# Kernel optimization log

Hardware: AMD Instinct MI355X
Metric: run time of the kernel (lower is better)

## Reference

```python
import jax, jax.numpy as jnp
import numpy as np

N = 100_000   # nodes
E = 800_000   # edges
F_IN = 128    # num_features
E_IN = 64     # edge_dim
H = 100       # n_hidden
L = 2         # num_gnn_layers
BN_EPS = 1e-5


def _lin(key, fan_in, fan_out, extra=()):
    kw, _ = jax.random.split(key)
    w = jax.random.normal(kw, (*extra, fan_in, fan_out), jnp.float32) / np.float32(np.sqrt(fan_in))
    b = jnp.zeros((*extra, fan_out), jnp.float32)
    return w, b


def setup_inputs() -> dict:
    key = jax.random.key(0)
    ks = jax.random.split(key, 12)
    x = jax.random.normal(ks[0], (N, F_IN), jnp.float32)
    edge_index = jax.random.randint(ks[1], (2, E), 0, N, dtype=jnp.int32)
    edge_attr = jax.random.normal(ks[2], (E, E_IN), jnp.float32)
    node_w, node_b = _lin(ks[3], F_IN, H)
    edge_w, edge_b = _lin(ks[4], E_IN, H)
    lin_w, lin_b = _lin(ks[5], H, H, (L,))   # GINEConv edge lin per layer
    w1, b1 = _lin(ks[6], H, H, (L,))         # GINEConv nn first Linear
    w2, b2 = _lin(ks[7], H, H, (L,))         # GINEConv nn second Linear
    gamma = jnp.ones((L, H), jnp.float32)
    beta = jnp.zeros((L, H), jnp.float32)
    ew1, eb1 = _lin(ks[8], 3 * H, H, (L,))   # edge-update MLP
    ew2, eb2 = _lin(ks[9], H, H, (L,))
    mw1, mb1 = _lin(ks[10], 3 * H, 50)
    k11, k12 = jax.random.split(ks[11])
    mw2, mb2 = _lin(k11, 50, 25)
    mw3, mb3 = _lin(k12, 25, 2)
    return dict(x=x, edge_index=edge_index, edge_attr=edge_attr,
                node_w=node_w, node_b=node_b, edge_w=edge_w, edge_b=edge_b,
                lin_w=lin_w, lin_b=lin_b, w1=w1, b1=b1, w2=w2, b2=b2,
                gamma=gamma, beta=beta, ew1=ew1, eb1=eb1, ew2=ew2, eb2=eb2,
                mw1=mw1, mb1=mb1, mw2=mw2, mb2=mb2, mw3=mw3, mb3=mb3)


def reference(x, edge_index, edge_attr, node_w, node_b, edge_w, edge_b,
              lin_w, lin_b, w1, b1, w2, b2, gamma, beta,
              ew1, eb1, ew2, eb2, mw1, mb1, mw2, mb2, mw3, mb3):
    src, dst = edge_index[0], edge_index[1]
    h = x @ node_w + node_b          # [N, H]
    e = edge_attr @ edge_w + edge_b  # [E, H]
    for i in range(L):
        # GINEConv: message = relu(x_src + lin(edge_attr)); sum-aggregate at dst
        msg = jax.nn.relu(h[src] + (e @ lin_w[i] + lin_b[i]))       # [E, H]
        agg = jax.ops.segment_sum(msg, dst, num_segments=N)         # [N, H]
        z = h + agg                                                  # (1+eps)*x + aggr, eps=0
        z = jax.nn.relu(z @ w1[i] + b1[i]) @ w2[i] + b2[i]
        # BatchNorm over nodes (training mode, biased variance)
        mu = z.mean(0)
        var = z.var(0)
        z = (z - mu) * jax.lax.rsqrt(var + BN_EPS) * gamma[i] + beta[i]
        h = (h + jax.nn.relu(z)) / 2
        # edge update: emlp(cat(x_src, x_dst, e))
        cat = jnp.concatenate([h[src], h[dst], e], axis=-1)         # [E, 3H]
        e = e + (jax.nn.relu(cat @ ew1[i] + eb1[i]) @ ew2[i] + eb2[i]) / 2
    feat = jnp.concatenate(
        [jax.nn.relu(jnp.concatenate([h[src], h[dst]], axis=-1)), e], axis=1)  # [E, 3H]
    out = jax.nn.relu(feat @ mw1 + mb1)
    out = jax.nn.relu(out @ mw2 + mb2)
    return out @ mw3 + mb3  # [E, 2]
```

## Files before the change

### kernel.cpp

```cpp
#include <hip/hip_runtime.h>

#define N_NODES 100000
#define N_EDGES 800000
#define HDIM 100
#define LDP 112
#define TSTR 104

typedef __attribute__((ext_vector_type(8))) short bf16x8;
typedef __attribute__((ext_vector_type(4))) float f32x4;

__device__ inline uint packsplit(float v) {
    uint u = __float_as_uint(v);
    float r = v - __uint_as_float(u & 0xFFFF0000u);
    return (u & 0xFFFF0000u) | (__float_as_uint(r) >> 16);
}
__device__ inline float recw(uint w) {
    return __uint_as_float(w & 0xFFFF0000u) + __uint_as_float(w << 16);
}
__device__ inline uint4 relu4(uint4 a) {
    a.x &= ~(uint)((int)a.x >> 31); a.y &= ~(uint)((int)a.y >> 31);
    a.z &= ~(uint)((int)a.z >> 31); a.w &= ~(uint)((int)a.w >> 31);
    return a;
}
__device__ inline void unpack16(uint4 a, uint4 b, bf16x8& h8, bf16x8& l8) {
    union { uint u[4]; bf16x8 v; } H, L;
    H.u[0] = __builtin_amdgcn_perm(a.y, a.x, 0x07060302u);
    H.u[1] = __builtin_amdgcn_perm(a.w, a.z, 0x07060302u);
    H.u[2] = __builtin_amdgcn_perm(b.y, b.x, 0x07060302u);
    H.u[3] = __builtin_amdgcn_perm(b.w, b.z, 0x07060302u);
    L.u[0] = __builtin_amdgcn_perm(a.y, a.x, 0x05040100u);
    L.u[1] = __builtin_amdgcn_perm(a.w, a.z, 0x05040100u);
    L.u[2] = __builtin_amdgcn_perm(b.y, b.x, 0x05040100u);
    L.u[3] = __builtin_amdgcn_perm(b.w, b.z, 0x05040100u);
    h8 = H.v; l8 = L.v;
}
__device__ inline void split8(float4 a, float4 b, bf16x8& h8, bf16x8& l8) {
    float v[8] = {a.x, a.y, a.z, a.w, b.x, b.y, b.z, b.w};
    bf16x8 hh, ll;
#pragma unroll
    for (int i = 0; i < 8; ++i) {
        uint u = __float_as_uint(v[i]);
        hh[i] = (short)(u >> 16);
        float r = v[i] - __uint_as_float(u & 0xFFFF0000u);
        ll[i] = (short)(__float_as_uint(r) >> 16);
    }
    h8 = hh; l8 = ll;
}

template<int CONCAT>
__global__ __launch_bounds__(256)
void pack_k(const float* __restrict__ W, ushort* __restrict__ hi, ushort* __restrict__ lo,
            int K, int NC, int Kpad, int NCpad, int total)
{
    int idx = blockIdx.x * 256 + threadIdx.x;
    if (idx >= total) return;
    int per = NCpad * Kpad;
    int b = idx / per, rem = idx - b * per;
    int col = rem / Kpad, kv = rem - col * Kpad;
    int srck; bool valid;
    if (CONCAT) {
        int seg = kv >> 7, off = kv & 127;
        srck = seg * 100 + off;
        valid = (off < 100) && (srck < K) && (col < NC);
    } else {
        srck = kv;
        valid = (kv < K) && (col < NC);
    }
    float v = valid ? W[(long)b * K * NC + (long)srck * NC + col] : 0.f;
    uint w = packsplit(v);
    hi[idx] = (ushort)(w >> 16);
    lo[idx] = (ushort)(w & 0xFFFFu);
}

template<int TILES, int TPW, int STEPS, int MODE, int GATHER, int AFP32, int OUTF32, int CLAMP>
__global__ __launch_bounds__(256, 2)
void gemm9_k(const uint* aP, int lda, const float* __restrict__ aF, int ldaf,
             const ushort* __restrict__ wH, const ushort* __restrict__ wL,
             const float* __restrict__ bias,
             float* __restrict__ Cf, uint* cP, int ldc,
             int M, int NC, const int* __restrict__ g0)
{
    constexpr int KPADW = STEPS * 32;
    const int tid  = threadIdx.x;
    const int lane = tid & 63;
    const int w    = tid >> 6;
    const int cl   = lane & 15;
    const int kgrp = lane >> 4;
    const long row0 = (long)blockIdx.x * 64;

    int arows[4];
#pragma unroll
    for (int rg = 0; rg < 4; ++rg) {
        long grow = row0 + rg * 16 + cl;
        int gc = (int)((grow < M) ? grow : (M - 1));
        arows[rg] = (GATHER == 3) ? g0[gc] : gc;
    }

    uint4  aw0[2][4], aw1[2][4];
    float4 af0[2][4], af1[2][4];
    bf16x8 bh[2][TPW], bl[2][TPW];
    f32x4  acc[TPW][4];
#pragma unroll
    for (int tp = 0; tp < TPW; ++tp)
#pragma unroll
        for (int rg = 0; rg < 4; ++rg) acc[tp][rg] = (f32x4){0.f, 0.f, 0.f, 0.f};

    auto loadA = [&](int st, int sl) {
        const int kk = st * 32 + kgrp * 8;
#pragma unroll
        for (int rg = 0; rg < 4; ++rg) {
            if (AFP32) {
                const float* p = aF + (size_t)arows[rg] * ldaf + kk;
                af0[sl][rg] = *(const float4*)p;
                af1[sl][rg] = *(const float4*)(p + 4);
            } else {
                bool ok = !CLAMP || ((st & 3) != 3) || (kgrp == 0);
                if (ok) {
                    const uint* p = aP + (size_t)arows[rg] * lda + kk;
                    aw0[sl][rg] = *(const uint4*)p;
                    aw1[sl][rg] = *(const uint4*)(p + 4);
                } else {
                    aw0[sl][rg] = make_uint4(0, 0, 0, 0);
                    aw1[sl][rg] = make_uint4(0, 0, 0, 0);
                }
            }
        }
    };
    auto loadB = [&](int st, int sl) {
        int kk = st * 32 + kgrp * 8;
#pragma unroll
        for (int tp = 0; tp < TPW; ++tp) {
            int colw = (w * TPW + tp) * 16 + cl;
            bh[sl][tp] = *(const bf16x8*)(wH + (size_t)colw * KPADW + kk);
            bl[sl][tp] = *(const bf16x8*)(wL + (size_t)colw * KPADW + kk);
        }
    };

    loadA(0, 0); loadB(0, 0);
    if (STEPS > 1) { loadA(1, 1); loadB(1, 1); }

#pragma unroll
    for (int st = 0; st < STEPS; ++st) {
        const int sl = st & 1;
#pragma unroll
        for (int rg = 0; rg < 4; ++rg) {
            bf16x8 aH, aL;
            if (AFP32) split8(af0[sl][rg], af1[sl][rg], aH, aL);
            else       unpack16(aw0[sl][rg], aw1[sl][rg], aH, aL);
#pragma unroll
            for (int tp = 0; tp < TPW; ++tp) {
                acc[tp][rg] = __builtin_amdgcn_mfma_f32_16x16x32_bf16(aL, bh[sl][tp], acc[tp][rg], 0, 0, 0);
                acc[tp][rg] = __builtin_amdgcn_mfma_f32_16x16x32_bf16(aH, bl[sl][tp], acc[tp][rg], 0, 0, 0);
                acc[tp][rg] = __builtin_amdgcn_mfma_f32_16x16x32_bf16(aH, bh[sl][tp], acc[tp][rg], 0, 0, 0);
            }
        }
        if (st + 2 < STEPS) { loadA(st + 2, sl); loadB(st + 2, sl); }
    }

#pragma unroll
    for (int tp = 0; tp < TPW; ++tp) {
        int col = (w * TPW + tp) * 16 + cl;
        if (col >= NC) continue;
        float bv = bias[col];
#pragma unroll
        for (int rg = 0; rg < 4; ++rg) {
#pragma unroll
            for (int i = 0; i < 4; ++i) {
                long grow = row0 + rg * 16 + kgrp * 4 + i;
                if (grow >= M) continue;
                float v = acc[tp][rg][i] + bv;
                if (MODE == 1) v = fmaxf(v, 0.f);
                long o = grow * (long)ldc + col;
                if (OUTF32) Cf[o] = v;
                else        cP[o] = packsplit(v);
            }
        }
    }
}

__global__ __launch_bounds__(256, 2)
void msg_agg_k(const uint* __restrict__ eP,
               const ushort* __restrict__ wH, const ushort* __restrict__ wL,
               const float* __restrict__ bias,
               const uint* __restrict__ hP,
               const int* __restrict__ psrc, const int* __restrict__ pdst,
               float* __restrict__ aggF)
{
    __shared__ float sm[64 * 108];
    __shared__ int sd[64];
    const int tid = threadIdx.x, lane = tid & 63, w = tid >> 6;
    const int cl = lane & 15, kgrp = lane >> 4;
    const long row0 = (long)blockIdx.x * 64;

    if (tid < 64) sd[tid] = pdst[row0 + tid];

    int sr[4][4];
#pragma unroll
    for (int rg = 0; rg < 4; ++rg)
#pragma unroll
        for (int i = 0; i < 4; ++i)
            sr[rg][i] = psrc[row0 + rg * 16 + kgrp * 4 + i];

    uint4 aw0[2][4], aw1[2][4];
    bf16x8 bh[2][2], bl[2][2];
    f32x4 acc[2][4];
#pragma unroll
    for (int tp = 0; tp < 2; ++tp)
#pragma unroll
        for (int rg = 0; rg < 4; ++rg) acc[tp][rg] = (f32x4){0.f, 0.f, 0.f, 0.f};

    auto loadA = [&](int st, int sl) {
        const int kk = st * 32 + kgrp * 8;
        bool ok = ((st & 3) != 3) || (kgrp == 0);
#pragma unroll
        for (int rg = 0; rg < 4; ++rg) {
            if (ok) {
                const uint* p = eP + (size_t)(row0 + rg * 16 + cl) * LDP + kk;
                aw0[sl][rg] = *(const uint4*)p;
                aw1[sl][rg] = *(const uint4*)(p + 4);
            } else {
                aw0[sl][rg] = make_uint4(0, 0, 0, 0);
                aw1[sl][rg] = make_uint4(0, 0, 0, 0);
            }
        }
    };
    auto loadB = [&](int st, int sl) {
        int kk = st * 32 + kgrp * 8;
#pragma unroll
        for (int tp = 0; tp < 2; ++tp) {
            int colw = (w * 2 + tp) * 16 + cl;
            bh[sl][tp] = *(const bf16x8*)(wH + (size_t)colw * 128 + kk);
            bl[sl][tp] = *(const bf16x8*)(wL + (size_t)colw * 128 + kk);
        }
    };

    loadA(0, 0); loadB(0, 0); loadA(1, 1); loadB(1, 1);
#pragma unroll
    for (int st = 0; st < 4; ++st) {
        const int sl = st & 1;
#pragma unroll
        for (int rg = 0; rg < 4; ++rg) {
            bf16x8 aH, aL;
            unpack16(aw0[sl][rg], aw1[sl][rg], aH, aL);
#pragma unroll
            for (int tp = 0; tp < 2; ++tp) {
                acc[tp][rg] = __builtin_amdgcn_mfma_f32_16x16x32_bf16(aL, bh[sl][tp], acc[tp][rg], 0, 0, 0);
                acc[tp][rg] = __builtin_amdgcn_mfma_f32_16x16x32_bf16(aH, bl[sl][tp], acc[tp][rg], 0, 0, 0);
                acc[tp][rg] = __builtin_amdgcn_mfma_f32_16x16x32_bf16(aH, bh[sl][tp], acc[tp][rg], 0, 0, 0);
            }
        }
        if (st + 2 < 4) { loadA(st + 2, sl); loadB(st + 2, sl); }
    }

#pragma unroll
    for (int tp = 0; tp < 2; ++tp) {
        int col = (w * 2 + tp) * 16 + cl;
        if (col < 100) {
            float bv = bias[col];
#pragma unroll
            for (int rg = 0; rg < 4; ++rg)
#pragma unroll
                for (int i = 0; i < 4; ++i) {
                    int row = rg * 16 + kgrp * 4 + i;
                    float hv = recw(hP[(size_t)sr[rg][i] * LDP + col]);
                    sm[row * 108 + col] = fmaxf(acc[tp][rg][i] + bv + hv, 0.f);
                }
        }
    }
    __syncthreads();

    if (tid < 100) {
        const int c = tid;
        int cur = sd[0];
        float s = 0.f;
        bool first = true;
        for (int r = 0; r < 64; ++r) {
            int d = sd[r];
            if (d != cur) {
                bool contPrev = first && (row0 > 0) && (pdst[row0 - 1] == cur);
                if (contPrev) atomicAdd(&aggF[(size_t)cur * TSTR + c], s);
                else aggF[(size_t)cur * TSTR + c] = recw(hP[(size_t)cur * LDP + c]) + s;
                first = false; s = 0.f; cur = d;
            }
            s += sm[r * 108 + c];
        }
        bool contPrev = first && (row0 > 0) && (pdst[row0 - 1] == cur);
        bool contNext = (row0 + 64 < N_EDGES) && (pdst[row0 + 64] == cur);
        if (contPrev || contNext) atomicAdd(&aggF[(size_t)cur * TSTR + c], s);
        else aggF[(size_t)cur * TSTR + c] = recw(hP[(size_t)cur * LDP + c]) + s;
    }
}

__global__ __launch_bounds__(256, 2)
void fused_edge_k(const uint* __restrict__ hP, uint* eP,
                  const ushort* __restrict__ w1H, const ushort* __restrict__ w1L,
                  const float* __restrict__ b1v,
                  const ushort* __restrict__ w2H, const ushort* __restrict__ w2L,
                  const float* __restrict__ b2v,
                  const int* __restrict__ g0, const int* __restrict__ g1)
{
    __shared__ uint sm[64 * 108];
    const int tid = threadIdx.x, lane = tid & 63, w = tid >> 6;
    const int cl = lane & 15, kgrp = lane >> 4;
    const long row0 = (long)blockIdx.x * 64;

    int rs[4], rd[4];
#pragma unroll
    for (int rg = 0; rg < 4; ++rg) {
        long gr = row0 + rg * 16 + cl;
        rs[rg] = g0[gr]; rd[rg] = g1[gr];
    }

    uint4 aw0[2][4], aw1[2][4];
    bf16x8 bh[2][2], bl[2][2];
    f32x4 acc[2][4];
#pragma unroll
    for (int tp = 0; tp < 2; ++tp)
#pragma unroll
        for (int rg = 0; rg < 4; ++rg) acc[tp][rg] = (f32x4){0.f, 0.f, 0.f, 0.f};

    auto loadA = [&](int st, int sl) {
        int seg = st >> 2, inseg = (st & 3) * 32 + kgrp * 8;
        bool ok = ((st & 3) != 3) || (kgrp == 0);
        const uint* base = (seg == 2) ? eP : hP;
#pragma unroll
        for (int rg = 0; rg < 4; ++rg) {
            if (ok) {
                long row = (seg == 0) ? rs[rg] : (seg == 1) ? rd[rg] : (row0 + rg * 16 + cl);
                const uint* p = base + (size_t)row * LDP + inseg;
                aw0[sl][rg] = *(const uint4*)p;
                aw1[sl][rg] = *(const uint4*)(p + 4);
            } else {
                aw0[sl][rg] = make_uint4(0, 0, 0, 0);
                aw1[sl][rg] = make_uint4(0, 0, 0, 0);
            }
        }
    };
    auto loadB = [&](int st, int sl) {
        int kk = st * 32 + kgrp * 8;
#pragma unroll
        for (int tp = 0; tp < 2; ++tp) {
            int colw = (w * 2 + tp) * 16 + cl;
            bh[sl][tp] = *(const bf16x8*)(w1H + (size_t)colw * 384 + kk);
            bl[sl][tp] = *(const bf16x8*)(w1L + (size_t)colw * 384 + kk);
        }
    };

    loadA(0, 0); loadB(0, 0); loadA(1, 1); loadB(1, 1);
#pragma unroll
    for (int st = 0; st < 12; ++st) {
        const int sl = st & 1;
#pragma unroll
        for (int rg = 0; rg < 4; ++rg) {
            bf16x8 aH, aL;
            unpack16(aw0[sl][rg], aw1[sl][rg], aH, aL);
#pragma unroll
            for (int tp = 0; tp < 2; ++tp) {
                acc[tp][rg] = __builtin_amdgcn_mfma_f32_16x16x32_bf16(aL, bh[sl][tp], acc[tp][rg], 0, 0, 0);
                acc[tp][rg] = __builtin_amdgcn_mfma_f32_16x16x32_bf16(aH, bl[sl][tp], acc[tp][rg], 0, 0, 0);
                acc[tp][rg] = __builtin_amdgcn_mfma_f32_16x16x32_bf16(aH, bh[sl][tp], acc[tp][rg], 0, 0, 0);
            }
        }
        if (st + 2 < 12) { loadA(st + 2, sl); loadB(st + 2, sl); }
    }

#pragma unroll
    for (int tp = 0; tp < 2; ++tp) {
        int col = (w * 2 + tp) * 16 + cl;
        if (col < 108) {
            float bv = (col < 100) ? b1v[col] : 0.f;
#pragma unroll
            for (int rg = 0; rg < 4; ++rg)
#pragma unroll
                for (int i = 0; i < 4; ++i) {
                    int row = rg * 16 + kgrp * 4 + i;
                    uint u = 0;
                    if (col < 100) u = packsplit(fmaxf(acc[tp][rg][i] + bv, 0.f));
                    sm[row * 108 + col] = u;
                }
        }
    }
    __syncthreads();

    f32x4 acc2[2][4];
#pragma unroll
    for (int tp = 0; tp < 2; ++tp)
#pragma unroll
        for (int rg = 0; rg < 4; ++rg) acc2[tp][rg] = (f32x4){0.f, 0.f, 0.f, 0.f};
    bf16x8 ch[2][2], clo[2][2];
    auto loadB2 = [&](int st, int sl) {
        int kk = st * 32 + kgrp * 8;
#pragma unroll
        for (int tp = 0; tp < 2; ++tp) {
            int colw = (w * 2 + tp) * 16 + cl;
            ch[sl][tp]  = *(const bf16x8*)(w2H + (size_t)colw * 128 + kk);
            clo[sl][tp] = *(const bf16x8*)(w2L + (size_t)colw * 128 + kk);
        }
    };
    loadB2(0, 0); loadB2(1, 1);
#pragma unroll
    for (int st = 0; st < 4; ++st) {
        const int sl = st & 1;
#pragma unroll
        for (int rg = 0; rg < 4; ++rg) {
            int row = rg * 16 + cl;
            int kk = st * 32 + kgrp * 8;
            uint4 q0 = make_uint4(0, 0, 0, 0), q1 = make_uint4(0, 0, 0, 0);
            if ((st != 3) || (kgrp == 0)) {
                q0 = *(const uint4*)&sm[row * 108 + kk];
                q1 = *(const uint4*)&sm[row * 108 + kk + 4];
            }
            bf16x8 aH, aL;
            unpack16(q0, q1, aH, aL);
#pragma unroll
            for (int tp = 0; tp < 2; ++tp) {
                acc2[tp][rg] = __builtin_amdgcn_mfma_f32_16x16x32_bf16(aL, ch[sl][tp], acc2[tp][rg], 0, 0, 0);
                acc2[tp][rg] = __builtin_amdgcn_mfma_f32_16x16x32_bf16(aH, clo[sl][tp], acc2[tp][rg], 0, 0, 0);
                acc2[tp][rg] = __builtin_amdgcn_mfma_f32_16x16x32_bf16(aH, ch[sl][tp], acc2[tp][rg], 0, 0, 0);
            }
        }
        if (st + 2 < 4) loadB2(st + 2, sl);
    }
#pragma unroll
    for (int tp = 0; tp < 2; ++tp) {
        int col = (w * 2 + tp) * 16 + cl;
        if (col >= 100) continue;
        float bv = b2v[col];
#pragma unroll
        for (int rg = 0; rg < 4; ++rg)
#pragma unroll
            for (int i = 0; i < 4; ++i) {
                long grow = row0 + rg * 16 + kgrp * 4 + i;
                long o = grow * (long)LDP + col;
                float v = recw(eP[o]) + 0.5f * (acc2[tp][rg][i] + bv);
                eP[o] = packsplit(v);
            }
    }
}

__global__ __launch_bounds__(256, 2)
void fused_final_k(const uint* __restrict__ hP, const uint* __restrict__ eP,
                   const ushort* __restrict__ m1H, const ushort* __restrict__ m1L,
                   const float* __restrict__ mb1,
                   const ushort* __restrict__ m2H, const ushort* __restrict__ m2L,
                   const float* __restrict__ mb2, const float* __restrict__ mw3,
                   const float* __restrict__ mb3,
                   const int* __restrict__ g0, const int* __restrict__ g1,
                   const int* __restrict__ eidx, float* __restrict__ out)
{
    __shared__ uint sm[64 * 68];
    const int tid = threadIdx.x, lane = tid & 63, w = tid >> 6;
    const int cl = lane & 15, kgrp = lane >> 4;
    const long row0 = (long)blockIdx.x * 64;

    int rs[4], rd[4];
#pragma unroll
    for (int rg = 0; rg < 4; ++rg) {
        long gr = row0 + rg * 16 + cl;
        rs[rg] = g0[gr]; rd[rg] = g1[gr];
    }

    uint4 aw0[2][4], aw1[2][4];
    bf16x8 bh[2], bl[2];
    f32x4 acc1[4];
#pragma unroll
    for (int rg = 0; rg < 4; ++rg) acc1[rg] = (f32x4){0.f, 0.f, 0.f, 0.f};

    auto loadA = [&](int st, int sl) {
        int seg = st >> 2, inseg = (st & 3) * 32 + kgrp * 8;
        bool ok = ((st & 3) != 3) || (kgrp == 0);
        const uint* base = (seg == 2) ? eP : hP;
#pragma unroll
        for (int rg = 0; rg < 4; ++rg) {
            if (ok) {
                long row = (seg == 0) ? rs[rg] : (seg == 1) ? rd[rg] : (row0 + rg * 16 + cl);
                const uint* p = base + (size_t)row * LDP + inseg;
                aw0[sl][rg] = *(const uint4*)p;
                aw1[sl][rg] = *(const uint4*)(p + 4);
            } else {
                aw0[sl][rg] = make_uint4(0, 0, 0, 0);
                aw1[sl][rg] = make_uint4(0, 0, 0, 0);
            }
        }
    };
    auto loadB = [&](int st, int sl) {
        int kk = st * 32 + kgrp * 8;
        int colw = w * 16 + cl;
        bh[sl] = *(const bf16x8*)(m1H + (size_t)colw * 384 + kk);
        bl[sl] = *(const bf16x8*)(m1L + (size_t)colw * 384 + kk);
    };

    loadA(0, 0); loadB(0, 0); loadA(1, 1); loadB(1, 1);
#pragma unroll
    for (int st = 0; st < 12; ++st) {
        const int sl = st & 1;
#pragma unroll
        for (int rg = 0; rg < 4; ++rg) {
            uint4 w0 = aw0[sl][rg], w1 = aw1[sl][rg];
            if (st < 8) { w0 = relu4(w0); w1 = relu4(w1); }
            bf16x8 aH, aL;
            unpack16(w0, w1, aH, aL);
            acc1[rg] = __builtin_amdgcn_mfma_f32_16x16x32_bf16(aL, bh[sl], acc1[rg], 0, 0, 0);
            acc1[rg] = __builtin_amdgcn_mfma_f32_16x16x32_bf16(aH, bl[sl], acc1[rg], 0, 0, 0);
            acc1[rg] = __builtin_amdgcn_mfma_f32_16x16x32_bf16(aH, bh[sl], acc1[rg], 0, 0, 0);
        }
        if (st + 2 < 12) { loadA(st + 2, sl); loadB(st + 2, sl); }
    }

    {
        int col = w * 16 + cl;
        float bv = (col < 50) ? mb1[col] : 0.f;
#pragma unroll
        for (int rg = 0; rg < 4; ++rg)
#pragma unroll
            for (int i = 0; i < 4; ++i) {
                int row = rg * 16 + kgrp * 4 + i;
                uint u = 0;
                if (col < 50) u = packsplit(fmaxf(acc1[rg][i] + bv, 0.f));
                sm[row * 68 + col] = u;
            }
    }
    __syncthreads();

    bf16x8 c2h[2][2], c2l[2][2];
#pragma unroll
    for (int t = 0; t < 2; ++t)
#pragma unroll
        for (int st = 0; st < 2; ++st) {
            long o = (long)(t * 16 + cl) * 64 + st * 32 + kgrp * 8;
            c2h[t][st] = *(const bf16x8*)(m2H + o);
            c2l[t][st] = *(const bf16x8*)(m2L + o);
        }
    const float bias0 = mb2[cl];
    const float bias1 = (cl + 16 < 25) ? mb2[cl + 16] : 0.f;
    const float w3a0 = mw3[cl * 2 + 0], w3a1 = mw3[cl * 2 + 1];
    const float w3b0 = (cl + 16 < 25) ? mw3[(cl + 16) * 2 + 0] : 0.f;
    const float w3b1 = (cl + 16 < 25) ? mw3[(cl + 16) * 2 + 1] : 0.f;
    const float b30 = mb3[0], b31 = mb3[1];

    const int row = w * 16 + cl;
    f32x4 a0 = (f32x4){0.f, 0.f, 0.f, 0.f}, a1 = a0;
#pragma unroll
    for (int st = 0; st < 2; ++st) {
        int kk = st * 32 + kgrp * 8;
        uint4 q0 = *(const uint4*)&sm[row * 68 + kk];
        uint4 q1 = *(const uint4*)&sm[row * 68 + kk + 4];
        bf16x8 aH, aL;
        unpack16(q0, q1, aH, aL);
        a0 = __builtin_amdgcn_mfma_f32_16x16x32_bf16(aL, c2h[0][st], a0, 0, 0, 0);
        a0 = __builtin_amdgcn_mfma_f32_16x16x32_bf16(aH, c2l[0][st], a0, 0, 0, 0);
        a0 = __builtin_amdgcn_mfma_f32_16x16x32_bf16(aH, c2h[0][st], a0, 0, 0, 0);
        a1 = __builtin_amdgcn_mfma_f32_16x16x32_bf16(aL, c2h[1][st], a1, 0, 0, 0);
        a1 = __builtin_amdgcn_mfma_f32_16x16x32_bf16(aH, c2l[1][st], a1, 0, 0, 0);
        a1 = __builtin_amdgcn_mfma_f32_16x16x32_bf16(aH, c2h[1][st], a1, 0, 0, 0);
    }
#pragma unroll
    for (int i = 0; i < 4; ++i) {
        float t0 = fmaxf(a0[i] + bias0, 0.f);
        float t1 = fmaxf(a1[i] + bias1, 0.f);
        float s0 = t0 * w3a0 + t1 * w3b0;
        float s1 = t0 * w3a1 + t1 * w3b1;
#pragma unroll
        for (int d = 1; d < 16; d <<= 1) {
            s0 += __shfl_xor(s0, d, 64);
            s1 += __shfl_xor(s1, d, 64);
        }
        if (cl == 0) {
            long grow = row0 + w * 16 + kgrp * 4 + i;
            int oe = eidx[grow];
            out[(long)oe * 2 + 0] = s0 + b30;
            out[(long)oe * 2 + 1] = s1 + b31;
        }
    }
}

__global__ __launch_bounds__(256)
void hist_k(const int* __restrict__ dst, int* __restrict__ cnt)
{
    int e = blockIdx.x * 256 + threadIdx.x;
    if (e < N_EDGES) atomicAdd(&cnt[dst[e]], 1);
}

__global__ __launch_bounds__(1024)
void scan_k(const int* __restrict__ cnt, int* __restrict__ off)
{
    __shared__ int part[1024];
    const int t = threadIdx.x;
    const int per = (N_NODES + 1023) / 1024;
    const int base = t * per;
    int s = 0;
    for (int i = 0; i < per; ++i) {
        int n = base + i;
        if (n < N_NODES) s += cnt[n];
    }
    part[t] = s;
    __syncthreads();
    for (int d = 1; d < 1024; d <<= 1) {
        int v = (t >= d) ? part[t - d] : 0;
        __syncthreads();
        part[t] += v;
        __syncthreads();
    }
    int run = (t == 0) ? 0 : part[t - 1];
    for (int i = 0; i < per; ++i) {
        int n = base + i;
        if (n < N_NODES) { off[n] = run; run += cnt[n]; }
    }
    if (t == 1023) off[N_NODES] = run;
}

__global__ __launch_bounds__(256)
void fill_k(const int* __restrict__ dst, const int* __restrict__ off,
            int* __restrict__ pos, int* __restrict__ eidx)
{
    int e = blockIdx.x * 256 + threadIdx.x;
    if (e >= N_EDGES) return;
    int d = dst[e];
    int p = atomicAdd(&pos[d], 1);
    eidx[off[d] + p] = e;
}

__global__ __launch_bounds__(256)
void perm_k(const int* __restrict__ eidx, const int* __restrict__ src,
            const int* __restrict__ dst, int* __restrict__ psrc, int* __restrict__ pdst)
{
    int j = blockIdx.x * 256 + threadIdx.x;
    if (j >= N_EDGES) return;
    int e = eidx[j];
    psrc[j] = src[e];
    pdst[j] = dst[e];
}

__global__ __launch_bounds__(256)
void h2agg_k(const uint* __restrict__ hP, float* __restrict__ aggF)
{
    unsigned idx = blockIdx.x * 256u + threadIdx.x;
    if (idx >= (unsigned)(N_NODES * 26)) return;
    unsigned n = idx / 26u;
    unsigned q = (idx - n * 26u) * 4u;
    long ob = (long)n * TSTR + q;
    if (q >= 100) {
        *(float4*)&aggF[ob] = make_float4(0.f, 0.f, 0.f, 0.f);
        return;
    }
    uint4 hw = *(const uint4*)&hP[(long)n * LDP + q];
    *(float4*)&aggF[ob] = make_float4(recw(hw.x), recw(hw.y), recw(hw.z), recw(hw.w));
}

__global__ __launch_bounds__(128)
void bn_stats_k(const float* __restrict__ z, float* __restrict__ stats)
{
    int c = threadIdx.x;
    if (c >= HDIM) return;
    long rows_per = (N_NODES + gridDim.x - 1) / gridDim.x;
    long r0 = (long)blockIdx.x * rows_per;
    long r1 = r0 + rows_per; if (r1 > N_NODES) r1 = N_NODES;
    float s = 0.f, s2 = 0.f;
    for (long r = r0; r < r1; ++r) {
        float v = z[r * TSTR + c];
        s += v; s2 += v * v;
    }
    atomicAdd(&stats[c], s);
    atomicAdd(&stats[HDIM + c], s2);
}

__global__ __launch_bounds__(256)
void bn_apply_k(const float* __restrict__ z2, const float* __restrict__ stats,
                const float* __restrict__ gamma, const float* __restrict__ beta,
                uint* __restrict__ hP)
{
    unsigned idx = blockIdx.x * 256u + threadIdx.x;
    if (idx >= (unsigned)(N_NODES * 25)) return;
    unsigned n = idx / 25u;
    unsigned q = (idx - n * 25u) * 4u;
    const float invN = 1.f / N_NODES;
    long ob = (long)n * LDP + q;
    uint4 hw = *(const uint4*)&hP[ob];
    float4 zv = *(const float4*)&z2[(long)n * TSTR + q];
    float hv[4] = {recw(hw.x), recw(hw.y), recw(hw.z), recw(hw.w)};
    float zz[4] = {zv.x, zv.y, zv.z, zv.w};
    float r[4];
#pragma unroll
    for (int i = 0; i < 4; ++i) {
        unsigned c = q + i;
        float mu  = stats[c] * invN;
        float var = stats[HDIM + c] * invN - mu * mu;
        float v = (zz[i] - mu) * rsqrtf(var + 1e-5f) * gamma[c] + beta[c];
        r[i] = (hv[i] + fmaxf(v, 0.f)) * 0.5f;
    }
    *(uint4*)&hP[ob] = make_uint4(packsplit(r[0]), packsplit(r[1]), packsplit(r[2]), packsplit(r[3]));
}

static inline int gb64(long m) { return (int)((m + 63) / 64); }

extern "C" void kernel_launch(void* const* d_in, const int* in_sizes, int n_in,
                              void* d_out, int out_size, void* d_ws, size_t ws_size,
                              hipStream_t stream)
{
    const float* x         = (const float*)d_in[0];
    const int*   ei        = (const int*)  d_in[1];
    const float* edge_attr = (const float*)d_in[2];
    const float* node_w    = (const float*)d_in[3];
    const float* node_b    = (const float*)d_in[4];
    const float* edge_w    = (const float*)d_in[5];
    const float* edge_b    = (const float*)d_in[6];
    const float* lin_w     = (const float*)d_in[7];
    const float* lin_b     = (const float*)d_in[8];
    const float* w1        = (const float*)d_in[9];
    const float* b1        = (const float*)d_in[10];
    const float* w2        = (const float*)d_in[11];
    const float* b2        = (const float*)d_in[12];
    const float* gamma     = (const float*)d_in[13];
    const float* beta      = (const float*)d_in[14];
    const float* ew1       = (const float*)d_in[15];
    const float* eb1       = (const float*)d_in[16];
    const float* ew2       = (const float*)d_in[17];
    const float* eb2       = (const float*)d_in[18];
    const float* mw1       = (const float*)d_in[19];
    const float* mb1       = (const float*)d_in[20];
    const float* mw2       = (const float*)d_in[21];
    const float* mb2       = (const float*)d_in[22];
    const float* mw3       = (const float*)d_in[23];
    const float* mb3       = (const float*)d_in[24];
    float* out = (float*)d_out;

    ushort* pw = (ushort*)d_ws;
    size_t off_w = 0;
    ushort *nwH, *nwL, *ewH, *ewL, *liH, *liL, *w1H, *w1L, *w2H, *w2L,
           *e1H, *e1L, *e2H, *e2L, *m1H, *m1L, *m2H, *m2L;
    auto nextw = [&](size_t s, ushort*& H, ushort*& L) { H = pw + off_w; L = pw + off_w + s; off_w += 2 * s; };
    nextw(128 * 128,     nwH, nwL);
    nextw(128 * 64,      ewH, ewL);
    nextw(2 * 128 * 128, liH, liL);
    nextw(2 * 128 * 128, w1H, w1L);
    nextw(2 * 128 * 128, w2H, w2L);
    nextw(2 * 128 * 384, e1H, e1L);
    nextw(2 * 128 * 128, e2H, e2L);
    nextw(64 * 384,      m1H, m1L);
    nextw(32 * 64,       m2H, m2L);

    int* intb = (int*)((char*)d_ws + (2u << 20));
    int* cnt   = intb;
    int* coff  = cnt + N_NODES;
    int* pos   = coff + N_NODES + 1;
    int* eidx  = pos + N_NODES;
    int* psrc  = eidx + N_EDGES;
    int* pdst  = psrc + N_EDGES;
    float* stats = (float*)(pdst + N_EDGES);

    char* fbase = (char*)d_ws + (16u << 20);
    uint* eP = (uint*)fbase;
    uint* hP = eP + (size_t)N_EDGES * LDP;
    uint* zP = hP + (size_t)N_NODES * LDP;
    char* big = (char*)(zP + (size_t)N_NODES * LDP);
    float* aggF = (float*)big;
    float* z2   = aggF + (size_t)N_NODES * TSTR;

    const int* srcp = ei;
    const int* dstp = ei + N_EDGES;
    dim3 blk(256);

    auto packl = [&](const float* W, ushort* H, ushort* L, int K, int NC, int Kp, int NCp, int batch, bool cc) {
        int total = batch * NCp * Kp;
        if (cc) pack_k<1><<<(total + 255) / 256, blk, 0, stream>>>(W, H, L, K, NC, Kp, NCp, total);
        else    pack_k<0><<<(total + 255) / 256, blk, 0, stream>>>(W, H, L, K, NC, Kp, NCp, total);
    };
    packl(node_w, nwH, nwL, 128, 100, 128, 128, 1, false);
    packl(edge_w, ewH, ewL,  64, 100,  64, 128, 1, false);
    packl(lin_w,  liH, liL, 100, 100, 128, 128, 2, false);
    packl(w1,     w1H, w1L, 100, 100, 128, 128, 2, false);
    packl(w2,     w2H, w2L, 100, 100, 128, 128, 2, false);
    packl(ew1,    e1H, e1L, 300, 100, 384, 128, 2, true);
    packl(ew2,    e2H, e2L, 100, 100, 128, 128, 2, false);
    packl(mw1,    m1H, m1L, 300,  50, 384,  64, 1, true);
    packl(mw2,    m2H, m2L,  50,  25,  64,  32, 1, false);

    hipMemsetAsync(cnt, 0, N_NODES * sizeof(int), stream);
    hist_k<<<(N_EDGES + 255) / 256, blk, 0, stream>>>(dstp, cnt);
    scan_k<<<1, dim3(1024), 0, stream>>>(cnt, coff);
    hipMemsetAsync(pos, 0, N_NODES * sizeof(int), stream);
    fill_k<<<(N_EDGES + 255) / 256, blk, 0, stream>>>(dstp, coff, pos, eidx);
    perm_k<<<(N_EDGES + 255) / 256, blk, 0, stream>>>(eidx, srcp, dstp, psrc, pdst);

    gemm9_k<8,2,4,0,0,1,0,0><<<gb64(N_NODES), blk, 0, stream>>>(
        nullptr, 0, x, 128, nwH, nwL, node_b, nullptr, hP, LDP, N_NODES, 100, nullptr);
    gemm9_k<8,2,2,0,3,1,0,0><<<gb64(N_EDGES), blk, 0, stream>>>(
        nullptr, 0, edge_attr, 64, ewH, ewL, edge_b, nullptr, eP, LDP, N_EDGES, 100, eidx);

    for (int i = 0; i < 2; ++i) {
        h2agg_k<<<(N_NODES * 26 + 255) / 256, blk, 0, stream>>>(hP, aggF);
        msg_agg_k<<<gb64(N_EDGES), blk, 0, stream>>>(
            eP, liH + (size_t)i * 16384, liL + (size_t)i * 16384, lin_b + i * HDIM,
            hP, psrc, pdst, aggF);
        gemm9_k<8,2,4,1,0,1,0,0><<<gb64(N_NODES), blk, 0, stream>>>(
            nullptr, 0, aggF, TSTR, w1H + (size_t)i * 16384, w1L + (size_t)i * 16384,
            b1 + i * HDIM, nullptr, zP, LDP, N_NODES, 100, nullptr);
        gemm9_k<8,2,4,0,0,0,1,1><<<gb64(N_NODES), blk, 0, stream>>>(
            zP, LDP, nullptr, 0, w2H + (size_t)i * 16384, w2L + (size_t)i * 16384,
            b2 + i * HDIM, z2, nullptr, TSTR, N_NODES, 100, nullptr);
        hipMemsetAsync(stats, 0, 2 * HDIM * sizeof(float), stream);
        bn_stats_k<<<1024, dim3(128), 0, stream>>>(z2, stats);
        bn_apply_k<<<(N_NODES * 25 + 255) / 256, blk, 0, stream>>>(
            z2, stats, gamma + i * HDIM, beta + i * HDIM, hP);
        fused_edge_k<<<gb64(N_EDGES), blk, 0, stream>>>(
            hP, eP,
            e1H + (size_t)i * 49152, e1L + (size_t)i * 49152, eb1 + i * HDIM,
            e2H + (size_t)i * 16384, e2L + (size_t)i * 16384, eb2 + i * HDIM,
            psrc, pdst);
    }

    fused_final_k<<<gb64(N_EDGES), blk, 0, stream>>>(
        hP, eP, m1H, m1L, mb1, m2H, m2L, mb2, mw3, mb3, psrc, pdst, eidx, out);
}
```

Baseline: 3.550 ms.

## Precompute per-node projections of src/dst blocks for edge MLP first layer

The first linear layer of the edge-update MLP and the final MLP is split by input block. The h[src] and h[dst] parts are computed once per node (N rows) into PSD/QSD tables, and the edge kernels only run a K=100 GEMM on the edge features plus two gathered adds. This removes two-thirds of the per-edge MFMA work and the gathered reads of full hidden rows, at the cost of extra node-level GEMM launches, new buffers and gathers from the projection tables. The relu on concatenated h in the final head is moved into the node GEMM through a new RELUA template flag.

Result: faster. 3.435 ms (-3.2%).

```diff
diff --git a/kernel.cpp b/kernel.cpp
--- a/kernel.cpp
+++ b/kernel.cpp
@@ -5,6 +5,9 @@
 #define HDIM 100
 #define LDP 112
 #define TSTR 104
+#define TS 108
+#define PSTR 224
+#define QSTR 128
 
 typedef __attribute__((ext_vector_type(8))) short bf16x8;
 typedef __attribute__((ext_vector_type(4))) float f32x4;
@@ -47,38 +50,29 @@
     h8 = hh; l8 = ll;
 }
 
-template<int CONCAT>
 __global__ __launch_bounds__(256)
 void pack_k(const float* __restrict__ W, ushort* __restrict__ hi, ushort* __restrict__ lo,
-            int K, int NC, int Kpad, int NCpad, int total)
+            int K, int NC, int Kpad, int NCpad, int total, int krow0, int srcK)
 {
     int idx = blockIdx.x * 256 + threadIdx.x;
     if (idx >= total) return;
     int per = NCpad * Kpad;
     int b = idx / per, rem = idx - b * per;
     int col = rem / Kpad, kv = rem - col * Kpad;
-    int srck; bool valid;
-    if (CONCAT) {
-        int seg = kv >> 7, off = kv & 127;
-        srck = seg * 100 + off;
-        valid = (off < 100) && (srck < K) && (col < NC);
-    } else {
-        srck = kv;
-        valid = (kv < K) && (col < NC);
-    }
-    float v = valid ? W[(long)b * K * NC + (long)srck * NC + col] : 0.f;
+    bool valid = (kv < K) && (col < NC);
+    float v = valid ? W[(long)b * srcK * NC + (long)(krow0 + kv) * NC + col] : 0.f;
     uint w = packsplit(v);
     hi[idx] = (ushort)(w >> 16);
     lo[idx] = (ushort)(w & 0xFFFFu);
 }
 
-template<int TILES, int TPW, int STEPS, int MODE, int GATHER, int AFP32, int OUTF32, int CLAMP>
+template<int TILES, int TPW, int STEPS, int MODE, int GATHER, int AFP32, int OUTF32, int CLAMP, int RELUA>
 __global__ __launch_bounds__(256, 2)
-void gemm9_k(const uint* aP, int lda, const float* __restrict__ aF, int ldaf,
-             const ushort* __restrict__ wH, const ushort* __restrict__ wL,
-             const float* __restrict__ bias,
-             float* __restrict__ Cf, uint* cP, int ldc,
-             int M, int NC, const int* __restrict__ g0)
+void gemm10_k(const uint* aP, int lda, const float* __restrict__ aF, int ldaf,
+              const ushort* __restrict__ wH, const ushort* __restrict__ wL,
+              const float* __restrict__ bias,
+              float* __restrict__ Cf, uint* cP, int ldc,
+              int M, int NC, const int* __restrict__ g0)
 {
     constexpr int KPADW = STEPS * 32;
     const int tid  = threadIdx.x;
@@ -146,7 +140,11 @@
         for (int rg = 0; rg < 4; ++rg) {
             bf16x8 aH, aL;
             if (AFP32) split8(af0[sl][rg], af1[sl][rg], aH, aL);
-            else       unpack16(aw0[sl][rg], aw1[sl][rg], aH, aL);
+            else {
+                uint4 q0 = aw0[sl][rg], q1 = aw1[sl][rg];
+                if (RELUA) { q0 = relu4(q0); q1 = relu4(q1); }
+                unpack16(q0, q1, aH, aL);
+            }
 #pragma unroll
             for (int tp = 0; tp < TPW; ++tp) {
                 acc[tp][rg] = __builtin_amdgcn_mfma_f32_16x16x32_bf16(aL, bh[sl][tp], acc[tp][rg], 0, 0, 0);
@@ -186,20 +184,14 @@
                const int* __restrict__ psrc, const int* __restrict__ pdst,
                float* __restrict__ aggF)
 {
-    __shared__ float sm[64 * 108];
-    __shared__ int sd[64];
+    __shared__ float sm[64 * TS];
+    __shared__ int sd[64], ssr[64];
     const int tid = threadIdx.x, lane = tid & 63, w = tid >> 6;
     const int cl = lane & 15, kgrp = lane >> 4;
     const long row0 = (long)blockIdx.x * 64;
 
-    if (tid < 64) sd[tid] = pdst[row0 + tid];
-
-    int sr[4][4];
-#pragma unroll
-    for (int rg = 0; rg < 4; ++rg)
-#pragma unroll
-        for (int i = 0; i < 4; ++i)
-            sr[rg][i] = psrc[row0 + rg * 16 + kgrp * 4 + i];
+    if (tid < 64) { sd[tid] = pdst[row0 + tid]; ssr[tid] = psrc[row0 + tid]; }
+    __syncthreads();
 
     uint4 aw0[2][4], aw1[2][4];
     bf16x8 bh[2][2], bl[2][2];
@@ -211,7 +203,7 @@
 
     auto loadA = [&](int st, int sl) {
         const int kk = st * 32 + kgrp * 8;
-        bool ok = ((st & 3) != 3) || (kgrp == 0);
+        bool ok = (st != 3) || (kgrp == 0);
 #pragma unroll
         for (int rg = 0; rg < 4; ++rg) {
             if (ok) {
@@ -262,8 +254,8 @@
 #pragma unroll
                 for (int i = 0; i < 4; ++i) {
                     int row = rg * 16 + kgrp * 4 + i;
-                    float hv = recw(hP[(size_t)sr[rg][i] * LDP + col]);
-                    sm[row * 108 + col] = fmaxf(acc[tp][rg][i] + bv + hv, 0.f);
+                    float hv = recw(hP[(size_t)ssr[row] * LDP + col]);
+                    sm[row * TS + col] = fmaxf(acc[tp][rg][i] + bv + hv, 0.f);
                 }
         }
     }
@@ -282,7 +274,7 @@
                 else aggF[(size_t)cur * TSTR + c] = recw(hP[(size_t)cur * LDP + c]) + s;
                 first = false; s = 0.f; cur = d;
             }
-            s += sm[r * 108 + c];
+            s += sm[r * TS + c];
         }
         bool contPrev = first && (row0 > 0) && (pdst[row0 - 1] == cur);
         bool contNext = (row0 + 64 < N_EDGES) && (pdst[row0 + 64] == cur);
@@ -292,24 +284,21 @@
 }
 
 __global__ __launch_bounds__(256, 2)
-void fused_edge_k(const uint* __restrict__ hP, uint* eP,
-                  const ushort* __restrict__ w1H, const ushort* __restrict__ w1L,
+void fused_edge_k(uint* eP, const uint* __restrict__ PSD,
+                  const ushort* __restrict__ weH, const ushort* __restrict__ weL,
                   const float* __restrict__ b1v,
                   const ushort* __restrict__ w2H, const ushort* __restrict__ w2L,
                   const float* __restrict__ b2v,
                   const int* __restrict__ g0, const int* __restrict__ g1)
 {
-    __shared__ uint sm[64 * 108];
+    __shared__ uint t0[64 * TS];
+    __shared__ int ssr[64], sdd[64];
     const int tid = threadIdx.x, lane = tid & 63, w = tid >> 6;
     const int cl = lane & 15, kgrp = lane >> 4;
     const long row0 = (long)blockIdx.x * 64;
 
-    int rs[4], rd[4];
-#pragma unroll
-    for (int rg = 0; rg < 4; ++rg) {
-        long gr = row0 + rg * 16 + cl;
-        rs[rg] = g0[gr]; rd[rg] = g1[gr];
-    }
+    if (tid < 64) { ssr[tid] = g0[row0 + tid]; sdd[tid] = g1[row0 + tid]; }
+    __syncthreads();
 
     uint4 aw0[2][4], aw1[2][4];
     bf16x8 bh[2][2], bl[2][2];
@@ -320,14 +309,12 @@
         for (int rg = 0; rg < 4; ++rg) acc[tp][rg] = (f32x4){0.f, 0.f, 0.f, 0.f};
 
     auto loadA = [&](int st, int sl) {
-        int seg = st >> 2, inseg = (st & 3) * 32 + kgrp * 8;
-        bool ok = ((st & 3) != 3) || (kgrp == 0);
-        const uint* base = (seg == 2) ? eP : hP;
+        const int kk = st * 32 + kgrp * 8;
+        bool ok = (st != 3) || (kgrp == 0);
 #pragma unroll
         for (int rg = 0; rg < 4; ++rg) {
             if (ok) {
-                long row = (seg == 0) ? rs[rg] : (seg == 1) ? rd[rg] : (row0 + rg * 16 + cl);
-                const uint* p = base + (size_t)row * LDP + inseg;
+                const uint* p = eP + (size_t)(row0 + rg * 16 + cl) * LDP + kk;
                 aw0[sl][rg] = *(const uint4*)p;
                 aw1[sl][rg] = *(const uint4*)(p + 4);
             } else {
@@ -336,19 +323,19 @@
             }
         }
     };
-    auto loadB = [&](int st, int sl) {
+    auto loadB1 = [&](int st, int sl) {
         int kk = st * 32 + kgrp * 8;
 #pragma unroll
         for (int tp = 0; tp < 2; ++tp) {
             int colw = (w * 2 + tp) * 16 + cl;
-            bh[sl][tp] = *(const bf16x8*)(w1H + (size_t)colw * 384 + kk);
-            bl[sl][tp] = *(const bf16x8*)(w1L + (size_t)colw * 384 + kk);
-        }
-    };
-
-    loadA(0, 0); loadB(0, 0); loadA(1, 1); loadB(1, 1);
-#pragma unroll
-    for (int st = 0; st < 12; ++st) {
+            bh[sl][tp] = *(const bf16x8*)(weH + (size_t)colw * 128 + kk);
+            bl[sl][tp] = *(const bf16x8*)(weL + (size_t)colw * 128 + kk);
+        }
+    };
+
+    loadA(0, 0); loadB1(0, 0); loadA(1, 1); loadB1(1, 1);
+#pragma unroll
+    for (int st = 0; st < 4; ++st) {
         const int sl = st & 1;
 #pragma unroll
         for (int rg = 0; rg < 4; ++rg) {
@@ -361,13 +348,13 @@
                 acc[tp][rg] = __builtin_amdgcn_mfma_f32_16x16x32_bf16(aH, bh[sl][tp], acc[tp][rg], 0, 0, 0);
             }
         }
-        if (st + 2 < 12) { loadA(st + 2, sl); loadB(st + 2, sl); }
+        if (st + 2 < 4) { loadA(st + 2, sl); loadB1(st + 2, sl); }
     }
 
 #pragma unroll
     for (int tp = 0; tp < 2; ++tp) {
         int col = (w * 2 + tp) * 16 + cl;
-        if (col < 108) {
+        if (col < TS) {
             float bv = (col < 100) ? b1v[col] : 0.f;
 #pragma unroll
             for (int rg = 0; rg < 4; ++rg)
@@ -375,8 +362,12 @@
                 for (int i = 0; i < 4; ++i) {
                     int row = rg * 16 + kgrp * 4 + i;
                     uint u = 0;
-                    if (col < 100) u = packsplit(fmaxf(acc[tp][rg][i] + bv, 0.f));
-                    sm[row * 108 + col] = u;
+                    if (col < 100) {
+                        float ps = recw(PSD[(size_t)ssr[row] * PSTR + col]);
+                        float pd = recw(PSD[(size_t)sdd[row] * PSTR + 112 + col]);
+                        u = packsplit(fmaxf(acc[tp][rg][i] + bv + ps + pd, 0.f));
+                    }
+                    t0[row * TS + col] = u;
                 }
         }
     }
@@ -403,12 +394,12 @@
         const int sl = st & 1;
 #pragma unroll
         for (int rg = 0; rg < 4; ++rg) {
-            int row = rg * 16 + cl;
             int kk = st * 32 + kgrp * 8;
             uint4 q0 = make_uint4(0, 0, 0, 0), q1 = make_uint4(0, 0, 0, 0);
             if ((st != 3) || (kgrp == 0)) {
-                q0 = *(const uint4*)&sm[row * 108 + kk];
-                q1 = *(const uint4*)&sm[row * 108 + kk + 4];
+                int ro = (rg * 16 + cl) * TS + kk;
+                q0 = *(const uint4*)&t0[ro];
+                q1 = *(const uint4*)&t0[ro + 4];
             }
             bf16x8 aH, aL;
             unpack16(q0, q1, aH, aL);
@@ -439,8 +430,8 @@
 }
 
 __global__ __launch_bounds__(256, 2)
-void fused_final_k(const uint* __restrict__ hP, const uint* __restrict__ eP,
-                   const ushort* __restrict__ m1H, const ushort* __restrict__ m1L,
+void fused_final_k(const uint* __restrict__ eP, const uint* __restrict__ QSD,
+                   const ushort* __restrict__ meH, const ushort* __restrict__ meL,
                    const float* __restrict__ mb1,
                    const ushort* __restrict__ m2H, const ushort* __restrict__ m2L,
                    const float* __restrict__ mb2, const float* __restrict__ mw3,
@@ -448,17 +439,14 @@
                    const int* __restrict__ g0, const int* __restrict__ g1,
                    const int* __restrict__ eidx, float* __restrict__ out)
 {
-    __shared__ uint sm[64 * 68];
+    __shared__ uint t0[64 * 68];
+    __shared__ int ssr[64], sdd[64];
     const int tid = threadIdx.x, lane = tid & 63, w = tid >> 6;
     const int cl = lane & 15, kgrp = lane >> 4;
     const long row0 = (long)blockIdx.x * 64;
 
-    int rs[4], rd[4];
-#pragma unroll
-    for (int rg = 0; rg < 4; ++rg) {
-        long gr = row0 + rg * 16 + cl;
-        rs[rg] = g0[gr]; rd[rg] = g1[gr];
-    }
+    if (tid < 64) { ssr[tid] = g0[row0 + tid]; sdd[tid] = g1[row0 + tid]; }
+    __syncthreads();
 
     uint4 aw0[2][4], aw1[2][4];
     bf16x8 bh[2], bl[2];
@@ -467,14 +455,12 @@
     for (int rg = 0; rg < 4; ++rg) acc1[rg] = (f32x4){0.f, 0.f, 0.f, 0.f};
 
     auto loadA = [&](int st, int sl) {
-        int seg = st >> 2, inseg = (st & 3) * 32 + kgrp * 8;
-        bool ok = ((st & 3) != 3) || (kgrp == 0);
-        const uint* base = (seg == 2) ? eP : hP;
+        const int kk = st * 32 + kgrp * 8;
+        bool ok = (st != 3) || (kgrp == 0);
 #pragma unroll
         for (int rg = 0; rg < 4; ++rg) {
             if (ok) {
-                long row = (seg == 0) ? rs[rg] : (seg == 1) ? rd[rg] : (row0 + rg * 16 + cl);
-                const uint* p = base + (size_t)row * LDP + inseg;
+                const uint* p = eP + (size_t)(row0 + rg * 16 + cl) * LDP + kk;
                 aw0[sl][rg] = *(const uint4*)p;
                 aw1[sl][rg] = *(const uint4*)(p + 4);
             } else {
@@ -483,28 +469,26 @@
             }
         }
     };
-    auto loadB = [&](int st, int sl) {
+    auto loadB1 = [&](int st, int sl) {
         int kk = st * 32 + kgrp * 8;
         int colw = w * 16 + cl;
-        bh[sl] = *(const bf16x8*)(m1H + (size_t)colw * 384 + kk);
-        bl[sl] = *(const bf16x8*)(m1L + (size_t)colw * 384 + kk);
-    };
-
-    loadA(0, 0); loadB(0, 0); loadA(1, 1); loadB(1, 1);
-#pragma unroll
-    for (int st = 0; st < 12; ++st) {
+        bh[sl] = *(const bf16x8*)(meH + (size_t)colw * 128 + kk);
+        bl[sl] = *(const bf16x8*)(meL + (size_t)colw * 128 + kk);
+    };
+
+    loadA(0, 0); loadB1(0, 0); loadA(1, 1); loadB1(1, 1);
+#pragma unroll
+    for (int st = 0; st < 4; ++st) {
         const int sl = st & 1;
 #pragma unroll
         for (int rg = 0; rg < 4; ++rg) {
-            uint4 w0 = aw0[sl][rg], w1 = aw1[sl][rg];
-            if (st < 8) { w0 = relu4(w0); w1 = relu4(w1); }
             bf16x8 aH, aL;
-            unpack16(w0, w1, aH, aL);
+            unpack16(aw0[sl][rg], aw1[sl][rg], aH, aL);
             acc1[rg] = __builtin_amdgcn_mfma_f32_16x16x32_bf16(aL, bh[sl], acc1[rg], 0, 0, 0);
             acc1[rg] = __builtin_amdgcn_mfma_f32_16x16x32_bf16(aH, bl[sl], acc1[rg], 0, 0, 0);
             acc1[rg] = __builtin_amdgcn_mfma_f32_16x16x32_bf16(aH, bh[sl], acc1[rg], 0, 0, 0);
         }
-        if (st + 2 < 12) { loadA(st + 2, sl); loadB(st + 2, sl); }
+        if (st + 2 < 4) { loadA(st + 2, sl); loadB1(st + 2, sl); }
     }
 
     {
@@ -516,8 +500,12 @@
             for (int i = 0; i < 4; ++i) {
                 int row = rg * 16 + kgrp * 4 + i;
                 uint u = 0;
-                if (col < 50) u = packsplit(fmaxf(acc1[rg][i] + bv, 0.f));
-                sm[row * 68 + col] = u;
+                if (col < 50) {
+                    float qs = recw(QSD[(size_t)ssr[row] * QSTR + col]);
+                    float qd = recw(QSD[(size_t)sdd[row] * QSTR + 64 + col]);
+                    u = packsplit(fmaxf(acc1[rg][i] + bv + qs + qd, 0.f));
+                }
+                t0[row * 68 + col] = u;
             }
     }
     __syncthreads();
@@ -543,8 +531,8 @@
 #pragma unroll
     for (int st = 0; st < 2; ++st) {
         int kk = st * 32 + kgrp * 8;
-        uint4 q0 = *(const uint4*)&sm[row * 68 + kk];
-        uint4 q1 = *(const uint4*)&sm[row * 68 + kk + 4];
+        uint4 q0 = *(const uint4*)&t0[row * 68 + kk];
+        uint4 q1 = *(const uint4*)&t0[row * 68 + kk + 4];
         bf16x8 aH, aL;
         unpack16(q0, q1, aH, aL);
         a0 = __builtin_amdgcn_mfma_f32_16x16x32_bf16(aL, c2h[0][st], a0, 0, 0, 0);
@@ -556,10 +544,10 @@
     }
 #pragma unroll
     for (int i = 0; i < 4; ++i) {
-        float t0 = fmaxf(a0[i] + bias0, 0.f);
-        float t1 = fmaxf(a1[i] + bias1, 0.f);
-        float s0 = t0 * w3a0 + t1 * w3b0;
-        float s1 = t0 * w3a1 + t1 * w3b1;
+        float t0v = fmaxf(a0[i] + bias0, 0.f);
+        float t1v = fmaxf(a1[i] + bias1, 0.f);
+        float s0 = t0v * w3a0 + t1v * w3b0;
+        float s1 = t0v * w3a1 + t1v * w3b1;
 #pragma unroll
         for (int d = 1; d < 16; d <<= 1) {
             s0 += __shfl_xor(s0, d, 64);
@@ -727,16 +715,21 @@
     ushort* pw = (ushort*)d_ws;
     size_t off_w = 0;
     ushort *nwH, *nwL, *ewH, *ewL, *liH, *liL, *w1H, *w1L, *w2H, *w2L,
-           *e1H, *e1L, *e2H, *e2L, *m1H, *m1L, *m2H, *m2L;
+           *wsH, *wsL, *wdH, *wdL, *weH, *weL, *e2H, *e2L,
+           *msH, *msL, *mdH, *mdL, *meH, *meL, *m2H, *m2L;
     auto nextw = [&](size_t s, ushort*& H, ushort*& L) { H = pw + off_w; L = pw + off_w + s; off_w += 2 * s; };
     nextw(128 * 128,     nwH, nwL);
     nextw(128 * 64,      ewH, ewL);
     nextw(2 * 128 * 128, liH, liL);
     nextw(2 * 128 * 128, w1H, w1L);
     nextw(2 * 128 * 128, w2H, w2L);
-    nextw(2 * 128 * 384, e1H, e1L);
+    nextw(2 * 128 * 128, wsH, wsL);
+    nextw(2 * 128 * 128, wdH, wdL);
+    nextw(2 * 128 * 128, weH, weL);
     nextw(2 * 128 * 128, e2H, e2L);
-    nextw(64 * 384,      m1H, m1L);
+    nextw(64 * 128,      msH, msL);
+    nextw(64 * 128,      mdH, mdL);
+    nextw(64 * 128,      meH, meL);
     nextw(32 * 64,       m2H, m2L);
 
     int* intb = (int*)((char*)d_ws + (2u << 20));
@@ -749,31 +742,36 @@
     float* stats = (float*)(pdst + N_EDGES);
 
     char* fbase = (char*)d_ws + (16u << 20);
-    uint* eP = (uint*)fbase;
-    uint* hP = eP + (size_t)N_EDGES * LDP;
-    uint* zP = hP + (size_t)N_NODES * LDP;
-    char* big = (char*)(zP + (size_t)N_NODES * LDP);
-    float* aggF = (float*)big;
+    uint* eP  = (uint*)fbase;
+    uint* hP  = eP + (size_t)N_EDGES * LDP;
+    uint* zP  = hP + (size_t)N_NODES * LDP;
+    uint* PSD = zP + (size_t)N_NODES * LDP;
+    uint* QSD = PSD + (size_t)N_NODES * PSTR;
+    float* aggF = (float*)(QSD + (size_t)N_NODES * QSTR);
     float* z2   = aggF + (size_t)N_NODES * TSTR;
 
     const int* srcp = ei;
     const int* dstp = ei + N_EDGES;
     dim3 blk(256);
 
-    auto packl = [&](const float* W, ushort* H, ushort* L, int K, int NC, int Kp, int NCp, int batch, bool cc) {
+    auto packl = [&](const float* W, ushort* H, ushort* L, int K, int NC, int Kp, int NCp,
+                     int batch, int krow0, int srcK) {
         int total = batch * NCp * Kp;
-        if (cc) pack_k<1><<<(total + 255) / 256, blk, 0, stream>>>(W, H, L, K, NC, Kp, NCp, total);
-        else    pack_k<0><<<(total + 255) / 256, blk, 0, stream>>>(W, H, L, K, NC, Kp, NCp, total);
-    };
-    packl(node_w, nwH, nwL, 128, 100, 128, 128, 1, false);
-    packl(edge_w, ewH, ewL,  64, 100,  64, 128, 1, false);
-    packl(lin_w,  liH, liL, 100, 100, 128, 128, 2, false);
-    packl(w1,     w1H, w1L, 100, 100, 128, 128, 2, false);
-    packl(w2,     w2H, w2L, 100, 100, 128, 128, 2, false);
-    packl(ew1,    e1H, e1L, 300, 100, 384, 128, 2, true);
-    packl(ew2,    e2H, e2L, 100, 100, 128, 128, 2, false);
-    packl(mw1,    m1H, m1L, 300,  50, 384,  64, 1, true);
-    packl(mw2,    m2H, m2L,  50,  25,  64,  32, 1, false);
+        pack_k<<<(total + 255) / 256, blk, 0, stream>>>(W, H, L, K, NC, Kp, NCp, total, krow0, srcK);
+    };
+    packl(node_w, nwH, nwL, 128, 100, 128, 128, 1, 0, 128);
+    packl(edge_w, ewH, ewL,  64, 100,  64, 128, 1, 0, 64);
+    packl(lin_w,  liH, liL, 100, 100, 128, 128, 2, 0, 100);
+    packl(w1,     w1H, w1L, 100, 100, 128, 128, 2, 0, 100);
+    packl(w2,     w2H, w2L, 100, 100, 128, 128, 2, 0, 100);
+    packl(ew1,    wsH, wsL, 100, 100, 128, 128, 2, 0,   300);
+    packl(ew1,    wdH, wdL, 100, 100, 128, 128, 2, 100, 300);
+    packl(ew1,    weH, weL, 100, 100, 128, 128, 2, 200, 300);
+    packl(ew2,    e2H, e2L, 100, 100, 128, 128, 2, 0, 100);
+    packl(mw1,    msH, msL, 100,  50, 128,  64, 1, 0,   300);
+    packl(mw1,    mdH, mdL, 100,  50, 128,  64, 1, 100, 300);
+    packl(mw1,    meH, meL, 100,  50, 128,  64, 1, 200, 300);
+    packl(mw2,    m2H, m2L,  50,  25,  64,  32, 1, 0, 50);
 
     hipMemsetAsync(cnt, 0, N_NODES * sizeof(int), stream);
     hist_k<<<(N_EDGES + 255) / 256, blk, 0, stream>>>(dstp, cnt);
@@ -782,33 +780,47 @@
     fill_k<<<(N_EDGES + 255) / 256, blk, 0, stream>>>(dstp, coff, pos, eidx);
     perm_k<<<(N_EDGES + 255) / 256, blk, 0, stream>>>(eidx, srcp, dstp, psrc, pdst);
 
-    gemm9_k<8,2,4,0,0,1,0,0><<<gb64(N_NODES), blk, 0, stream>>>(
+    gemm10_k<8,2,4,0,0,1,0,0,0><<<gb64(N_NODES), blk, 0, stream>>>(
         nullptr, 0, x, 128, nwH, nwL, node_b, nullptr, hP, LDP, N_NODES, 100, nullptr);
-    gemm9_k<8,2,2,0,3,1,0,0><<<gb64(N_EDGES), blk, 0, stream>>>(
+    gemm10_k<8,2,2,0,3,1,0,0,0><<<gb64(N_EDGES), blk, 0, stream>>>(
         nullptr, 0, edge_attr, 64, ewH, ewL, edge_b, nullptr, eP, LDP, N_EDGES, 100, eidx);
 
+    float zerob[1]; (void)zerob;
     for (int i = 0; i < 2; ++i) {
         h2agg_k<<<(N_NODES * 26 + 255) / 256, blk, 0, stream>>>(hP, aggF);
         msg_agg_k<<<gb64(N_EDGES), blk, 0, stream>>>(
             eP, liH + (size_t)i * 16384, liL + (size_t)i * 16384, lin_b + i * HDIM,
             hP, psrc, pdst, aggF);
-        gemm9_k<8,2,4,1,0,1,0,0><<<gb64(N_NODES), blk, 0, stream>>>(
+        gemm10_k<8,2,4,1,0,1,0,0,0><<<gb64(N_NODES), blk, 0, stream>>>(
             nullptr, 0, aggF, TSTR, w1H + (size_t)i * 16384, w1L + (size_t)i * 16384,
             b1 + i * HDIM, nullptr, zP, LDP, N_NODES, 100, nullptr);
-        gemm9_k<8,2,4,0,0,0,1,1><<<gb64(N_NODES), blk, 0, stream>>>(
+        gemm10_k<8,2,4,0,0,0,1,1,0><<<gb64(N_NODES), blk, 0, stream>>>(
             zP, LDP, nullptr, 0, w2H + (size_t)i * 16384, w2L + (size_t)i * 16384,
             b2 + i * HDIM, z2, nullptr, TSTR, N_NODES, 100, nullptr);
         hipMemsetAsync(stats, 0, 2 * HDIM * sizeof(float), stream);
         bn_stats_k<<<1024, dim3(128), 0, stream>>>(z2, stats);
         bn_apply_k<<<(N_NODES * 25 + 255) / 256, blk, 0, stream>>>(
             z2, stats, gamma + i * HDIM, beta + i * HDIM, hP);
+        hipMemsetAsync(stats + 2 * HDIM, 0, 128 * sizeof(float), stream);
+        gemm10_k<8,2,4,0,0,0,0,1,0><<<gb64(N_NODES), blk, 0, stream>>>(
+            hP, LDP, nullptr, 0, wsH + (size_t)i * 16384, wsL + (size_t)i * 16384,
+            stats + 2 * HDIM, nullptr, PSD, PSTR, N_NODES, 100, nullptr);
+        gemm10_k<8,2,4,0,0,0,0,1,0><<<gb64(N_NODES), blk, 0, stream>>>(
+            hP, LDP, nullptr, 0, wdH + (size_t)i * 16384, wdL + (size_t)i * 16384,
+            stats + 2 * HDIM, nullptr, PSD + 112, PSTR, N_NODES, 100, nullptr);
         fused_edge_k<<<gb64(N_EDGES), blk, 0, stream>>>(
-            hP, eP,
-            e1H + (size_t)i * 49152, e1L + (size_t)i * 49152, eb1 + i * HDIM,
+            eP, PSD,
+            weH + (size_t)i * 16384, weL + (size_t)i * 16384, eb1 + i * HDIM,
             e2H + (size_t)i * 16384, e2L + (size_t)i * 16384, eb2 + i * HDIM,
             psrc, pdst);
     }
 
+    hipMemsetAsync(stats + 2 * HDIM, 0, 128 * sizeof(float), stream);
+    gemm10_k<4,1,4,0,0,0,0,1,1><<<gb64(N_NODES), blk, 0, stream>>>(
+        hP, LDP, nullptr, 0, msH, msL, stats + 2 * HDIM, nullptr, QSD, QSTR, N_NODES, 50, nullptr);
+    gemm10_k<4,1,4,0,0,0,0,1,1><<<gb64(N_NODES), blk, 0, stream>>>(
+        hP, LDP, nullptr, 0, mdH, mdL, stats + 2 * HDIM, nullptr, QSD + 64, QSTR, N_NODES, 50, nullptr);
+
     fused_final_k<<<gb64(N_EDGES), blk, 0, stream>>>(
-        hP, eP, m1H, m1L, mb1, m2H, m2L, mb2, mw3, mb3, psrc, pdst, eidx, out);
-}
+        eP, QSD, meH, meL, mb1, m2H, m2L, mb2, mw3, mb3, psrc, pdst, eidx, out);
+}
```
